# Kernel tuning notes

Hardware: AMD Instinct MI355X
Metric: run time of the kernel (lower is better)

The kernel has to match this reference:

```python
import jax, jax.numpy as jnp
import numpy as np

N_NODES = 100000
N_EDGES = 1600000
F_IN = 128
HID = 128
N_GRAPHS = 1024


def setup_inputs() -> dict:
    key = jax.random.key(0)
    ks = jax.random.split(key, 20)
    x = jax.random.normal(ks[0], (N_NODES, F_IN), dtype=jnp.float32)
    edge_index = jax.random.randint(ks[1], (2, N_EDGES), 0, N_NODES, dtype=jnp.int64)
    batch = jnp.sort(jax.random.randint(ks[2], (N_NODES,), 0, N_GRAPHS, dtype=jnp.int64))
    def lin(k, fi, fo):
        s = 1.0 / np.sqrt(fi)
        return jax.random.uniform(k, (fi, fo), jnp.float32, -s, s)
    params = {
        'W1': lin(ks[3], F_IN, HID), 'b1': jnp.zeros((HID,), jnp.float32),
        'W2': lin(ks[4], HID, HID), 'b2': jnp.zeros((HID,), jnp.float32),
        'W3': lin(ks[5], HID, HID), 'b3': jnp.zeros((HID,), jnp.float32),
        'W4': lin(ks[6], HID, HID), 'b4': jnp.zeros((HID,), jnp.float32),
        'W5': lin(ks[7], HID, HID), 'b5': jnp.zeros((HID,), jnp.float32),
        'beta1': jnp.ones((1,), jnp.float32),
        'beta2': jnp.ones((1,), jnp.float32),
        'Wl': lin(ks[8], HID, 1), 'bl': jnp.zeros((1,), jnp.float32),
    }
    return {'x': x, 'edge_index': edge_index, 'batch': batch, **params}


def _forward(x, src, dst, batch, W1, b1, W2, b2, W3, b3, W4, b4, W5, b5, beta1, beta2, Wl, bl):
    N = x.shape[0]
    # symmetric GCN normalization over A + I (shared by all GCNConv layers)
    deg = jax.ops.segment_sum(jnp.ones_like(dst, dtype=x.dtype), dst, num_segments=N)
    d_is = jnp.where(deg > 0, jax.lax.rsqrt(deg), 0.0)
    norm = d_is[src] * d_is[dst]  # [E+N]

    def gcn(h, W, b):
        m = (h @ W)[src] * norm[:, None]          # per-edge messages
        return jax.ops.segment_sum(m, dst, num_segments=N) + b

    def agnn(h, beta):
        nrm = jnp.maximum(jnp.linalg.norm(h, axis=1, keepdims=True), 1e-12)
        hn = h / nrm
        alpha = beta[0] * jnp.sum(hn[src] * hn[dst], axis=1)  # cosine sim per edge
        amax = jax.ops.segment_max(alpha, dst, num_segments=N)
        e = jnp.exp(alpha - amax[dst])
        denom = jax.ops.segment_sum(e, dst, num_segments=N)
        w = e / denom[dst]
        return jax.ops.segment_sum(h[src] * w[:, None], dst, num_segments=N)

    h = jnp.tanh(gcn(x, W1, b1))
    h = jnp.tanh(gcn(h, W2, b2))
    h = jnp.tanh(gcn(h, W3, b3))
    h = jnp.tanh(gcn(h, W4, b4))
    h = jnp.tanh(gcn(h, W5, b5))
    h = jnp.tanh(agnn(h, beta1))
    h = jnp.tanh(agnn(h, beta2))

    # global mean pool per graph
    sums = jax.ops.segment_sum(h, batch, num_segments=N_GRAPHS)
    cnts = jax.ops.segment_sum(jnp.ones((N,), h.dtype), batch, num_segments=N_GRAPHS)
    pooled = sums / jnp.maximum(cnts, 1.0)[:, None]

    # layer_norm over feature dim, no affine
    mu = jnp.mean(pooled, axis=-1, keepdims=True)
    var = jnp.mean(jnp.square(pooled - mu), axis=-1, keepdims=True)
    ln = (pooled - mu) * jax.lax.rsqrt(var + 1e-5)
    # dropout is identity in eval mode
    return ln @ Wl + bl


def reference(x, edge_index, batch, W1, b1, W2, b2, W3, b3, W4, b4, W5, b5, beta1, beta2, Wl, bl):
    N = x.shape[0]
    loops = jnp.arange(N, dtype=edge_index.dtype)
    src = jnp.concatenate([edge_index[0], loops])  # add self-loops (GCNConv & AGNNConv default)
    dst = jnp.concatenate([edge_index[1], loops])
    return _forward(x, src, dst, batch, W1, b1, W2, b2, W3, b3, W4, b4, W5, b5, beta1, beta2, Wl, bl)
```

## Files before the change

### kernel.cpp

```cpp
#include <hip/hip_runtime.h>
#include <hip/hip_fp16.h>
#include <math.h>

typedef _Float16 f16x8 __attribute__((ext_vector_type(8)));
typedef _Float16 f16x2 __attribute__((ext_vector_type(2)));
typedef float f32x4 __attribute__((ext_vector_type(4)));

union U4H8 { uint4 u; f16x8 h; };
union U4D2 { uint4 u; f16x2 d2[4]; unsigned w[4]; };

__device__ __forceinline__ float fmamix_lo(unsigned pk, float s, float acc) {
    asm("v_fma_mix_f32 %0, %1, %2, %0 op_sel:[0,0,0] op_sel_hi:[1,0,0]"
        : "+v"(acc) : "v"(pk), "v"(s));
    return acc;
}
__device__ __forceinline__ float fmamix_hi(unsigned pk, float s, float acc) {
    asm("v_fma_mix_f32 %0, %1, %2, %0 op_sel:[1,0,0] op_sel_hi:[1,0,0]"
        : "+v"(acc) : "v"(pk), "v"(s));
    return acc;
}
__device__ __forceinline__ float fdot2(f16x2 a, f16x2 b, float c) {
#if __has_builtin(__builtin_amdgcn_fdot2)
    return __builtin_amdgcn_fdot2(a, b, c, false);
#else
    asm("v_dot2_f32_f16 %0, %1, %2, %0" : "+v"(c) : "v"(a), "v"(b));
    return c;
#endif
}

__device__ __forceinline__ void unpack8(uint4 u, float* f) {
    union { uint4 u; __half2 h2[4]; } U; U.u = u;
    float2 a = __half22float2(U.h2[0]);
    float2 b = __half22float2(U.h2[1]);
    float2 c = __half22float2(U.h2[2]);
    float2 d = __half22float2(U.h2[3]);
    f[0] = a.x; f[1] = a.y; f[2] = b.x; f[3] = b.y;
    f[4] = c.x; f[5] = c.y; f[6] = d.x; f[7] = d.y;
}

__global__ void k_zero(int* p, int n) {
    int i = blockIdx.x * blockDim.x + threadIdx.x;
    if (i < n) p[i] = 0;
}

__global__ void k_count(const int* __restrict__ dst, int* deg4, int* rank, int E, int N) {
    int i = blockIdx.x * blockDim.x + threadIdx.x;
    if (i < E) rank[i] = atomicAdd(&deg4[(i & 3) * N + dst[i]], 1);
}

__global__ void k_meta_pre(const int* __restrict__ deg4, int* deg, float* dis, int N) {
    int n = blockIdx.x * blockDim.x + threadIdx.x;
    if (n >= N) return;
    int d = deg4[n] + deg4[N + n] + deg4[2 * N + n] + deg4[3 * N + n];
    deg[n] = d;
    dis[n] = rsqrtf((float)(d + 1));
}

__global__ void k_meta_post(const int* __restrict__ deg4, const int* __restrict__ offs,
                            int4* meta, int N) {
    int n = blockIdx.x * blockDim.x + threadIdx.x;
    if (n >= N) return;
    int d0 = deg4[n], d1 = deg4[N + n], d2 = deg4[2 * N + n];
    meta[n] = make_int4(offs[n] + 1, d0, d0 + d1, d0 + d1 + d2);
}

__global__ void k_scan1(const int* __restrict__ deg, int* part, int N) {
    int base = blockIdx.x * 1024;
    int tid = threadIdx.x;
    int s = 0;
#pragma unroll
    for (int j = 0; j < 4; ++j) {
        int idx = base + tid * 4 + j;
        if (idx < N) s += deg[idx] + 1;
    }
    __shared__ int sm[256];
    sm[tid] = s;
    __syncthreads();
    for (int off = 128; off > 0; off >>= 1) {
        if (tid < off) sm[tid] += sm[tid + off];
        __syncthreads();
    }
    if (tid == 0) part[blockIdx.x] = sm[0];
}

__global__ void k_scan2(int* part, int nb, int* offs, int N) {
    if (blockIdx.x == 0 && threadIdx.x == 0) {
        int run = 0;
        for (int b = 0; b < nb; ++b) { int t = part[b]; part[b] = run; run += t; }
        offs[N] = run;
    }
}

__global__ void k_scan3(const int* __restrict__ deg, const int* __restrict__ part,
                        int* offs, int N) {
    __shared__ int sm[256];
    int base = blockIdx.x * 1024;
    int tid = threadIdx.x;
    int a[4];
    int s = 0;
#pragma unroll
    for (int j = 0; j < 4; ++j) {
        int idx = base + tid * 4 + j;
        a[j] = (idx < N) ? (deg[idx] + 1) : 0;
        s += a[j];
    }
    sm[tid] = s;
    __syncthreads();
    for (int off = 1; off < 256; off <<= 1) {
        int v = (tid >= off) ? sm[tid - off] : 0;
        __syncthreads();
        sm[tid] += v;
        __syncthreads();
    }
    int excl = sm[tid] - s + part[blockIdx.x];
#pragma unroll
    for (int j = 0; j < 4; ++j) {
        int idx = base + tid * 4 + j;
        if (idx < N) offs[idx] = excl;
        excl += a[j];
    }
}

__global__ void k_fill(const int* __restrict__ ei, int E, int N,
                       const int4* __restrict__ meta,
                       const int* __restrict__ rank, int* csr) {
    int i = blockIdx.x * blockDim.x + threadIdx.x;
    if (i < E) {
        int s = ei[i], d = ei[E + i];
        int c = i & 3;
        int4 m = meta[d];
        int base = (c == 0) ? 0 : ((c == 1) ? m.y : ((c == 2) ? m.z : m.w));
        csr[m.x + base + rank[i]] = s;
    } else if (i < E + N) {
        int n = i - E;
        csr[meta[n].x - 1] = n;
    }
}

__global__ void k_gstart(const int* __restrict__ batch, int N, int* gstart, int G) {
    int g = blockIdx.x * blockDim.x + threadIdx.x;
    if (g > G) return;
    int lo = 0, hi = N;
    while (lo < hi) {
        int mid = (lo + hi) >> 1;
        if (batch[mid] < g) lo = mid + 1; else hi = mid;
    }
    gstart[g] = lo;
}

__global__ __launch_bounds__(256) void k_cast(
    const float* __restrict__ x, const float* __restrict__ dis,
    __half* __restrict__ hx, int npairs)
{
    int i = blockIdx.x * blockDim.x + threadIdx.x;
    if (i >= npairs) return;
    float2 v = ((const float2*)x)[i];
    float d = dis[i >> 6];
    ((__half2*)hx)[i] = __floats2half2_rn(d * v.x, d * v.y);
}

__global__ void k_prepw(const float* __restrict__ W, __half* __restrict__ wt_hi,
                        __half* __restrict__ wt_lo) {
    int t = blockIdx.x * 256 + threadIdx.x;
    int j = t & 7, q = t >> 3;
    int l15 = q & 15, nt = (q >> 4) & 7;
    int lg = (q >> 7) & 3, ks = q >> 9;
    int n = nt * 16 + l15, k = ks * 32 + lg * 8 + j;
    float w = W[k * 128 + n];
    __half hi = __float2half_rn(w);
    wt_hi[t] = hi;
    wt_lo[t] = __float2half_rn(w - __half2float(hi));
}

__global__ __launch_bounds__(256) void k_gcn_agg(
    const __half* __restrict__ g, const int* __restrict__ csr,
    const int* __restrict__ offs, const float* __restrict__ dis,
    __half* __restrict__ agg, int N)
{
    int node = (blockIdx.x * blockDim.x + threadIdx.x) >> 4;
    int l = threadIdx.x & 15;
    if (node >= N) return;
    int j0 = offs[node], j1 = offs[node + 1];
    float dd = dis[node];
    const uint4* h4 = (const uint4*)g;
    float one = 1.0f;
    float acc[8] = {0.f, 0.f, 0.f, 0.f, 0.f, 0.f, 0.f, 0.f};
    int j = j0;
    for (; j + 8 <= j1; j += 8) {
        U4D2 u[8];
#pragma unroll
        for (int e = 0; e < 8; ++e) {
            int s = csr[j + e];
            u[e].u = h4[(unsigned)(s * 16 + l)];
        }
#pragma unroll
        for (int e = 0; e < 8; ++e)
#pragma unroll
            for (int k = 0; k < 4; ++k) {
                acc[2 * k]     = fmamix_lo(u[e].w[k], one, acc[2 * k]);
                acc[2 * k + 1] = fmamix_hi(u[e].w[k], one, acc[2 * k + 1]);
            }
    }
    for (; j + 4 <= j1; j += 4) {
        U4D2 u[4];
#pragma unroll
        for (int e = 0; e < 4; ++e) {
            int s = csr[j + e];
            u[e].u = h4[(unsigned)(s * 16 + l)];
        }
#pragma unroll
        for (int e = 0; e < 4; ++e)
#pragma unroll
            for (int k = 0; k < 4; ++k) {
                acc[2 * k]     = fmamix_lo(u[e].w[k], one, acc[2 * k]);
                acc[2 * k + 1] = fmamix_hi(u[e].w[k], one, acc[2 * k + 1]);
            }
    }
    for (; j < j1; ++j) {
        int s = csr[j];
        U4D2 u; u.u = h4[(unsigned)(s * 16 + l)];
#pragma unroll
        for (int k = 0; k < 4; ++k) {
            acc[2 * k]     = fmamix_lo(u.w[k], one, acc[2 * k]);
            acc[2 * k + 1] = fmamix_hi(u.w[k], one, acc[2 * k + 1]);
        }
    }
    union { uint4 u; __half2 h2[4]; } P;
    P.h2[0] = __floats2half2_rn(dd * acc[0], dd * acc[1]);
    P.h2[1] = __floats2half2_rn(dd * acc[2], dd * acc[3]);
    P.h2[2] = __floats2half2_rn(dd * acc[4], dd * acc[5]);
    P.h2[3] = __floats2half2_rn(dd * acc[6], dd * acc[7]);
    ((uint4*)agg)[(unsigned)(node * 16 + l)] = P.u;
}

#define GEMM_STG_OFF 65536
#define GEMM_STG_STRIDE 72
#define GEMM_LDS_BYTES (65536 + 8 * 16 * GEMM_STG_STRIDE)

__global__ __launch_bounds__(512) void k_gemm_mfma(
    const __half* __restrict__ in, const __half* __restrict__ wt_hi,
    const __half* __restrict__ wt_lo, const float* __restrict__ bias,
    const float* __restrict__ scale, __half* __restrict__ out,
    int ntiles, int nrows, float* __restrict__ invn_out)
{
    extern __shared__ char smem[];
    uint4* wlds = (uint4*)smem;
    int tid = threadIdx.x;
    int wv = tid >> 6;
    char* stg = smem + GEMM_STG_OFF + wv * 16 * GEMM_STG_STRIDE;

    {
        const uint4* sh = (const uint4*)wt_hi;
        const uint4* sl = (const uint4*)wt_lo;
        for (int t = tid; t < 2048; t += 512) {
            wlds[t] = sh[t];
            wlds[t + 2048] = sl[t];
        }
    }
    __syncthreads();

    int lane = tid & 63;
    int l15 = lane & 15, lg = lane >> 4;

    f32x4 bv[8];
#pragma unroll
    for (int nt = 0; nt < 8; ++nt)
        bv[nt] = *(const f32x4*)(bias + nt * 16 + lg * 4);

    int wid = blockIdx.x * 8 + wv;
    int t0 = wid * 2;
    for (int tile = t0; tile < t0 + 2 && tile < ntiles; ++tile) {
        int row0 = tile * 16;
        int row = row0 + l15;
        if (row >= nrows) row = nrows - 1;

        U4H8 b[4];
        const uint4* ap = (const uint4*)(in + (size_t)row * 128);
#pragma unroll
        for (int ks = 0; ks < 4; ++ks) b[ks].u = ap[ks * 4 + lg];

        f32x4 acc[8];
#pragma unroll
        for (int nt = 0; nt < 8; ++nt) acc[nt] = (f32x4){0.f, 0.f, 0.f, 0.f};

#pragma unroll
        for (int ks = 0; ks < 4; ++ks) {
#pragma unroll
            for (int nt = 0; nt < 8; ++nt) {
                int fi = (ks * 4 + lg) * 128 + nt * 16 + l15;
                U4H8 ah; ah.u = wlds[fi];
                U4H8 al; al.u = wlds[fi + 2048];
                acc[nt] = __builtin_amdgcn_mfma_f32_16x16x32_f16(ah.h, b[ks].h, acc[nt], 0, 0, 0);
                acc[nt] = __builtin_amdgcn_mfma_f32_16x16x32_f16(al.h, b[ks].h, acc[nt], 0, 0, 0);
            }
        }

        float sc = scale ? scale[row] : 1.0f;
        float sq = 0.f;
        int node = lane >> 2, sub = lane & 3;
#pragma unroll
        for (int np = 0; np < 4; ++np) {
#pragma unroll
            for (int h = 0; h < 2; ++h) {
                int nt = np * 2 + h;
                float o[4];
#pragma unroll
                for (int r = 0; r < 4; ++r) {
                    float xv = acc[nt][r] + bv[nt][r];
                    float e = __expf(xv + xv);
                    o[r] = 1.f - 2.f / (e + 1.f);
                    sq += o[r] * o[r];
                }
                union { __half2 h2[2]; uint2 u; } pk;
                pk.h2[0] = __floats2half2_rn(sc * o[0], sc * o[1]);
                pk.h2[1] = __floats2half2_rn(sc * o[2], sc * o[3]);
                *(uint2*)(stg + l15 * GEMM_STG_STRIDE + h * 32 + lg * 8) = pk.u;
            }
            uint4 v = *(const uint4*)(stg + node * GEMM_STG_STRIDE + sub * 16);
            if (row0 + node < nrows)
                *(uint4*)(out + (size_t)(row0 + node) * 128 + np * 32 + sub * 8) = v;
        }
        if (invn_out) {
            sq += __shfl_xor(sq, 16, 64);
            sq += __shfl_xor(sq, 32, 64);
            if (lg == 0) invn_out[row] = 1.0f / fmaxf(sqrtf(sq), 1e-12f);
        }
    }
}

__global__ __launch_bounds__(256) void k_agnn(
    const __half* __restrict__ h, const int* __restrict__ csr,
    const int* __restrict__ offs, const float* __restrict__ invn,
    const float* __restrict__ beta_p, __half* __restrict__ out, int N,
    float* __restrict__ invn_out)
{
    int node = (blockIdx.x * blockDim.x + threadIdx.x) >> 4;
    int l = threadIdx.x & 15;
    if (node >= N) return;
    int j0 = offs[node], j1 = offs[node + 1];
    const uint4* h4 = (const uint4*)h;
    U4D2 D; D.u = h4[(unsigned)(node * 16 + l)];
    float bi = beta_p[0] * invn[node];
    float denom = 0.f;
    float acc[8] = {0.f, 0.f, 0.f, 0.f, 0.f, 0.f, 0.f, 0.f};
    int j = j0;
    for (; j + 4 <= j1; j += 4) {
        U4D2 A[4];
        float in_[4];
#pragma unroll
        for (int e = 0; e < 4; ++e) {
            int s = csr[j + e];
            in_[e] = invn[s];
            A[e].u = h4[(unsigned)(s * 16 + l)];
        }
        float d[4] = {0.f, 0.f, 0.f, 0.f};
#pragma unroll
        for (int e = 0; e < 4; ++e)
#pragma unroll
            for (int k = 0; k < 4; ++k) d[e] = fdot2(A[e].d2[k], D.d2[k], d[e]);
#pragma unroll
        for (int off = 1; off < 16; off <<= 1) {
            d[0] += __shfl_xor(d[0], off, 64);
            d[1] += __shfl_xor(d[1], off, 64);
            d[2] += __shfl_xor(d[2], off, 64);
            d[3] += __shfl_xor(d[3], off, 64);
        }
        float p[4];
#pragma unroll
        for (int e = 0; e < 4; ++e) {
            p[e] = __expf(bi * in_[e] * d[e]);
            denom += p[e];
        }
#pragma unroll
        for (int e = 0; e < 4; ++e)
#pragma unroll
            for (int k = 0; k < 4; ++k) {
                acc[2 * k]     = fmamix_lo(A[e].w[k], p[e], acc[2 * k]);
                acc[2 * k + 1] = fmamix_hi(A[e].w[k], p[e], acc[2 * k + 1]);
            }
    }
    for (; j < j1; ++j) {
        int s = csr[j];
        float ins = invn[s];
        U4D2 A; A.u = h4[(unsigned)(s * 16 + l)];
        float d = 0.f;
#pragma unroll
        for (int k = 0; k < 4; ++k) d = fdot2(A.d2[k], D.d2[k], d);
#pragma unroll
        for (int off = 1; off < 16; off <<= 1) d += __shfl_xor(d, off, 64);
        float p = __expf(bi * ins * d);
        denom += p;
#pragma unroll
        for (int k = 0; k < 4; ++k) {
            acc[2 * k]     = fmamix_lo(A.w[k], p, acc[2 * k]);
            acc[2 * k + 1] = fmamix_hi(A.w[k], p, acc[2 * k + 1]);
        }
    }
    float inv = 1.0f / denom;
    float o[8];
#pragma unroll
    for (int i = 0; i < 8; ++i) o[i] = tanhf(acc[i] * inv);
    union { uint4 u; __half2 h2[4]; } P;
    P.h2[0] = __floats2half2_rn(o[0], o[1]);
    P.h2[1] = __floats2half2_rn(o[2], o[3]);
    P.h2[2] = __floats2half2_rn(o[4], o[5]);
    P.h2[3] = __floats2half2_rn(o[6], o[7]);
    ((uint4*)out)[(unsigned)(node * 16 + l)] = P.u;
    if (invn_out) {
        float s2 = 0.f;
#pragma unroll
        for (int i = 0; i < 8; ++i) s2 += o[i] * o[i];
#pragma unroll
        for (int off = 1; off < 16; off <<= 1) s2 += __shfl_xor(s2, off, 64);
        if (l == 0) invn_out[node] = 1.0f / fmaxf(sqrtf(s2), 1e-12f);
    }
}

__global__ __launch_bounds__(256) void k_pool(
    const __half* __restrict__ h, const int* __restrict__ gstart,
    const float* __restrict__ Wl, const float* __restrict__ bl,
    float* __restrict__ out, int G)
{
    int g = (blockIdx.x * blockDim.x + threadIdx.x) >> 4;
    int l = threadIdx.x & 15;
    if (g >= G) return;
    int s = gstart[g], e = gstart[g + 1];
    const uint4* hp = (const uint4*)h + l;
    float acc[8] = {0.f, 0.f, 0.f, 0.f, 0.f, 0.f, 0.f, 0.f};
    for (int n = s; n < e; ++n) {
        float f[8]; unpack8(hp[(size_t)n * 16], f);
#pragma unroll
        for (int i = 0; i < 8; ++i) acc[i] += f[i];
    }
    float inv = 1.0f / fmaxf((float)(e - s), 1.0f);
#pragma unroll
    for (int i = 0; i < 8; ++i) acc[i] *= inv;
    float part = 0.f;
#pragma unroll
    for (int i = 0; i < 8; ++i) part += acc[i];
#pragma unroll
    for (int off = 1; off < 16; off <<= 1) part += __shfl_xor(part, off, 64);
    float mu = part * (1.0f / 128.0f);
    float vpart = 0.f;
#pragma unroll
    for (int i = 0; i < 8; ++i) { float d = acc[i] - mu; vpart += d * d; }
#pragma unroll
    for (int off = 1; off < 16; off <<= 1) vpart += __shfl_xor(vpart, off, 64);
    float r = rsqrtf(vpart * (1.0f / 128.0f) + 1e-5f);
    float4 w0 = *(const float4*)(Wl + l * 8);
    float4 w1 = *(const float4*)(Wl + l * 8 + 4);
    float wv[8] = {w0.x, w0.y, w0.z, w0.w, w1.x, w1.y, w1.z, w1.w};
    float dot = 0.f;
#pragma unroll
    for (int i = 0; i < 8; ++i) dot += (acc[i] - mu) * r * wv[i];
#pragma unroll
    for (int off = 1; off < 16; off <<= 1) dot += __shfl_xor(dot, off, 64);
    if (l == 0) out[g] = dot + bl[0];
}

extern "C" void kernel_launch(void* const* d_in, const int* in_sizes, int n_in,
                              void* d_out, int out_size, void* d_ws, size_t ws_size,
                              hipStream_t stream) {
    const float* x  = (const float*)d_in[0];
    const int* ei   = (const int*)d_in[1];
    const int* batch = (const int*)d_in[2];
    const float* Ws[5] = {(const float*)d_in[3], (const float*)d_in[5],
                          (const float*)d_in[7], (const float*)d_in[9],
                          (const float*)d_in[11]};
    const float* bs[5] = {(const float*)d_in[4], (const float*)d_in[6],
                          (const float*)d_in[8], (const float*)d_in[10],
                          (const float*)d_in[12]};
    const float* beta1 = (const float*)d_in[13];
    const float* beta2 = (const float*)d_in[14];
    const float* Wl = (const float*)d_in[15];
    const float* bl = (const float*)d_in[16];
    float* out = (float*)d_out;

    int N = in_sizes[0] / 128;
    int E = in_sizes[1] / 2;
    int G = out_size;

    char* ws = (char*)d_ws;
    size_t off = 0;
    auto alloc = [&](size_t bytes) -> void* {
        void* p = ws + off;
        off = (off + bytes + 255) & ~(size_t)255;
        return p;
    };
    __half* aggh = (__half*)alloc((size_t)N * 128 * 2);
    __half* hA   = (__half*)alloc((size_t)N * 128 * 2);
    __half* hB   = (__half*)alloc((size_t)N * 128 * 2);
    int*   deg4  = (int*)alloc((size_t)4 * N * 4);
    int*   deg   = (int*)alloc((size_t)N * 4);
    int*   offs  = (int*)alloc((size_t)(N + 1) * 4);
    int4*  meta  = (int4*)alloc((size_t)N * 16);
    int*   rank  = (int*)alloc((size_t)E * 4);
    int*   csr   = (int*)alloc((size_t)(E + N) * 4);
    float* dis   = (float*)alloc((size_t)N * 4);
    float* invn  = (float*)alloc((size_t)N * 4);
    float* invn2 = (float*)alloc((size_t)N * 4);
    __half* wtHi = (__half*)alloc((size_t)5 * 16384 * 2);
    __half* wtLo = (__half*)alloc((size_t)5 * 16384 * 2);
    int nb = (N + 1023) / 1024;
    int*   part  = (int*)alloc((size_t)nb * 4);
    int*   gst   = (int*)alloc((size_t)(G + 1) * 4);

    k_zero<<<(4 * N + 255) / 256, 256, 0, stream>>>(deg4, 4 * N);
    k_count<<<(E + 255) / 256, 256, 0, stream>>>(ei + E, deg4, rank, E, N);
    k_meta_pre<<<(N + 255) / 256, 256, 0, stream>>>(deg4, deg, dis, N);
    k_scan1<<<nb, 256, 0, stream>>>(deg, part, N);
    k_scan2<<<1, 64, 0, stream>>>(part, nb, offs, N);
    k_scan3<<<nb, 256, 0, stream>>>(deg, part, offs, N);
    k_meta_post<<<(N + 255) / 256, 256, 0, stream>>>(deg4, offs, meta, N);
    k_fill<<<(E + N + 255) / 256, 256, 0, stream>>>(ei, E, N, meta, rank, csr);
    k_gstart<<<(G + 1 + 255) / 256, 256, 0, stream>>>(batch, N, gst, G);
    k_cast<<<(N * 64 + 255) / 256, 256, 0, stream>>>(x, dis, hA, N * 64);
    for (int l = 0; l < 5; ++l)
        k_prepw<<<64, 256, 0, stream>>>(Ws[l], wtHi + l * 16384, wtLo + l * 16384);

    int aggBlocks = (N + 15) / 16;
    int ntiles = (N + 15) / 16;
    int gemmBlocks = (ntiles + 15) / 16;

    const __half* hin = hA;
    __half* hout = hB;
    for (int l = 0; l < 5; ++l) {
        k_gcn_agg<<<aggBlocks, 256, 0, stream>>>(hin, csr, offs, dis, aggh, N);
        k_gemm_mfma<<<gemmBlocks, 512, GEMM_LDS_BYTES, stream>>>(
            aggh, wtHi + l * 16384, wtLo + l * 16384, bs[l],
            (l < 4) ? dis : nullptr, hout, ntiles, N,
            (l == 4) ? invn : nullptr);
        const __half* t = hin; hin = hout; hout = (__half*)t;
    }
    k_agnn<<<aggBlocks, 256, 0, stream>>>(hin, csr, offs, invn, beta1, hout, N, invn2);
    k_agnn<<<aggBlocks, 256, 0, stream>>>(hout, csr, offs, invn2, beta2, (__half*)hin, N, nullptr);
    k_pool<<<(G + 15) / 16, 256, 0, stream>>>(hin, gst, Wl, bl, out, G);
}
```

Before: 725.1 us.

## Fuse GCN neighbor aggregation into the MFMA GEMM kernel

```diff
diff --git a/kernel.cpp b/kernel.cpp
--- a/kernel.cpp
+++ b/kernel.cpp
@@ -172,76 +172,16 @@
     wt_lo[t] = __float2half_rn(w - __half2float(hi));
 }
 
-__global__ __launch_bounds__(256) void k_gcn_agg(
-    const __half* __restrict__ g, const int* __restrict__ csr,
-    const int* __restrict__ offs, const float* __restrict__ dis,
-    __half* __restrict__ agg, int N)
-{
-    int node = (blockIdx.x * blockDim.x + threadIdx.x) >> 4;
-    int l = threadIdx.x & 15;
-    if (node >= N) return;
-    int j0 = offs[node], j1 = offs[node + 1];
-    float dd = dis[node];
-    const uint4* h4 = (const uint4*)g;
-    float one = 1.0f;
-    float acc[8] = {0.f, 0.f, 0.f, 0.f, 0.f, 0.f, 0.f, 0.f};
-    int j = j0;
-    for (; j + 8 <= j1; j += 8) {
-        U4D2 u[8];
-#pragma unroll
-        for (int e = 0; e < 8; ++e) {
-            int s = csr[j + e];
-            u[e].u = h4[(unsigned)(s * 16 + l)];
-        }
-#pragma unroll
-        for (int e = 0; e < 8; ++e)
-#pragma unroll
-            for (int k = 0; k < 4; ++k) {
-                acc[2 * k]     = fmamix_lo(u[e].w[k], one, acc[2 * k]);
-                acc[2 * k + 1] = fmamix_hi(u[e].w[k], one, acc[2 * k + 1]);
-            }
-    }
-    for (; j + 4 <= j1; j += 4) {
-        U4D2 u[4];
-#pragma unroll
-        for (int e = 0; e < 4; ++e) {
-            int s = csr[j + e];
-            u[e].u = h4[(unsigned)(s * 16 + l)];
-        }
-#pragma unroll
-        for (int e = 0; e < 4; ++e)
-#pragma unroll
-            for (int k = 0; k < 4; ++k) {
-                acc[2 * k]     = fmamix_lo(u[e].w[k], one, acc[2 * k]);
-                acc[2 * k + 1] = fmamix_hi(u[e].w[k], one, acc[2 * k + 1]);
-            }
-    }
-    for (; j < j1; ++j) {
-        int s = csr[j];
-        U4D2 u; u.u = h4[(unsigned)(s * 16 + l)];
-#pragma unroll
-        for (int k = 0; k < 4; ++k) {
-            acc[2 * k]     = fmamix_lo(u.w[k], one, acc[2 * k]);
-            acc[2 * k + 1] = fmamix_hi(u.w[k], one, acc[2 * k + 1]);
-        }
-    }
-    union { uint4 u; __half2 h2[4]; } P;
-    P.h2[0] = __floats2half2_rn(dd * acc[0], dd * acc[1]);
-    P.h2[1] = __floats2half2_rn(dd * acc[2], dd * acc[3]);
-    P.h2[2] = __floats2half2_rn(dd * acc[4], dd * acc[5]);
-    P.h2[3] = __floats2half2_rn(dd * acc[6], dd * acc[7]);
-    ((uint4*)agg)[(unsigned)(node * 16 + l)] = P.u;
-}
-
 #define GEMM_STG_OFF 65536
 #define GEMM_STG_STRIDE 72
 #define GEMM_LDS_BYTES (65536 + 8 * 16 * GEMM_STG_STRIDE)
 
-__global__ __launch_bounds__(512) void k_gemm_mfma(
-    const __half* __restrict__ in, const __half* __restrict__ wt_hi,
-    const __half* __restrict__ wt_lo, const float* __restrict__ bias,
-    const float* __restrict__ scale, __half* __restrict__ out,
-    int ntiles, int nrows, float* __restrict__ invn_out)
+__global__ __launch_bounds__(512) void k_gcn_fused(
+    const __half* __restrict__ h, const int* __restrict__ csr,
+    const int* __restrict__ offs, const float* __restrict__ dis,
+    const __half* __restrict__ wt_hi, const __half* __restrict__ wt_lo,
+    const float* __restrict__ bias, const float* __restrict__ scale,
+    __half* __restrict__ out, int ntiles, int nrows, float* __restrict__ invn_out)
 {
     extern __shared__ char smem[];
     uint4* wlds = (uint4*)smem;
@@ -261,6 +201,8 @@
 
     int lane = tid & 63;
     int l15 = lane & 15, lg = lane >> 4;
+    const uint4* h4 = (const uint4*)h;
+    float one = 1.0f;
 
     f32x4 bv[8];
 #pragma unroll
@@ -274,15 +216,55 @@
         int row = row0 + l15;
         if (row >= nrows) row = nrows - 1;
 
+        float ag[32];
+#pragma unroll
+        for (int i = 0; i < 32; ++i) ag[i] = 0.f;
+        int j0 = offs[row], j1 = offs[row + 1];
+        int j = j0;
+        for (; j + 2 <= j1; j += 2) {
+            int s0 = csr[j], s1 = csr[j + 1];
+            U4D2 c0[4], c1[4];
+#pragma unroll
+            for (int ks = 0; ks < 4; ++ks) c0[ks].u = h4[(unsigned)(s0 * 16 + ks * 4 + lg)];
+#pragma unroll
+            for (int ks = 0; ks < 4; ++ks) c1[ks].u = h4[(unsigned)(s1 * 16 + ks * 4 + lg)];
+#pragma unroll
+            for (int ks = 0; ks < 4; ++ks)
+#pragma unroll
+                for (int w = 0; w < 4; ++w) {
+                    ag[ks * 8 + 2 * w]     = fmamix_lo(c0[ks].w[w], one, ag[ks * 8 + 2 * w]);
+                    ag[ks * 8 + 2 * w + 1] = fmamix_hi(c0[ks].w[w], one, ag[ks * 8 + 2 * w + 1]);
+                    ag[ks * 8 + 2 * w]     = fmamix_lo(c1[ks].w[w], one, ag[ks * 8 + 2 * w]);
+                    ag[ks * 8 + 2 * w + 1] = fmamix_hi(c1[ks].w[w], one, ag[ks * 8 + 2 * w + 1]);
+                }
+        }
+        for (; j < j1; ++j) {
+            int s = csr[j];
+            U4D2 c[4];
+#pragma unroll
+            for (int ks = 0; ks < 4; ++ks) c[ks].u = h4[(unsigned)(s * 16 + ks * 4 + lg)];
+#pragma unroll
+            for (int ks = 0; ks < 4; ++ks)
+#pragma unroll
+                for (int w = 0; w < 4; ++w) {
+                    ag[ks * 8 + 2 * w]     = fmamix_lo(c[ks].w[w], one, ag[ks * 8 + 2 * w]);
+                    ag[ks * 8 + 2 * w + 1] = fmamix_hi(c[ks].w[w], one, ag[ks * 8 + 2 * w + 1]);
+                }
+        }
+        float dd = dis[row];
         U4H8 b[4];
-        const uint4* ap = (const uint4*)(in + (size_t)row * 128);
-#pragma unroll
-        for (int ks = 0; ks < 4; ++ks) b[ks].u = ap[ks * 4 + lg];
+#pragma unroll
+        for (int ks = 0; ks < 4; ++ks) {
+            union { uint4 u; __half2 h2[4]; } P;
+#pragma unroll
+            for (int w = 0; w < 4; ++w)
+                P.h2[w] = __floats2half2_rn(dd * ag[ks * 8 + 2 * w], dd * ag[ks * 8 + 2 * w + 1]);
+            b[ks].u = P.u;
+        }
 
         f32x4 acc[8];
 #pragma unroll
         for (int nt = 0; nt < 8; ++nt) acc[nt] = (f32x4){0.f, 0.f, 0.f, 0.f};
-
 #pragma unroll
         for (int ks = 0; ks < 4; ++ks) {
 #pragma unroll
@@ -301,8 +283,8 @@
 #pragma unroll
         for (int np = 0; np < 4; ++np) {
 #pragma unroll
-            for (int h = 0; h < 2; ++h) {
-                int nt = np * 2 + h;
+            for (int hh = 0; hh < 2; ++hh) {
+                int nt = np * 2 + hh;
                 float o[4];
 #pragma unroll
                 for (int r = 0; r < 4; ++r) {
@@ -314,7 +296,7 @@
                 union { __half2 h2[2]; uint2 u; } pk;
                 pk.h2[0] = __floats2half2_rn(sc * o[0], sc * o[1]);
                 pk.h2[1] = __floats2half2_rn(sc * o[2], sc * o[3]);
-                *(uint2*)(stg + l15 * GEMM_STG_STRIDE + h * 32 + lg * 8) = pk.u;
+                *(uint2*)(stg + l15 * GEMM_STG_STRIDE + hh * 32 + lg * 8) = pk.u;
             }
             uint4 v = *(const uint4*)(stg + node * GEMM_STG_STRIDE + sub * 16);
             if (row0 + node < nrows)
@@ -487,7 +469,6 @@
         off = (off + bytes + 255) & ~(size_t)255;
         return p;
     };
-    __half* aggh = (__half*)alloc((size_t)N * 128 * 2);
     __half* hA   = (__half*)alloc((size_t)N * 128 * 2);
     __half* hB   = (__half*)alloc((size_t)N * 128 * 2);
     int*   deg4  = (int*)alloc((size_t)4 * N * 4);
@@ -520,14 +501,13 @@
 
     int aggBlocks = (N + 15) / 16;
     int ntiles = (N + 15) / 16;
-    int gemmBlocks = (ntiles + 15) / 16;
+    int fusedBlocks = (ntiles + 15) / 16;
 
     const __half* hin = hA;
     __half* hout = hB;
     for (int l = 0; l < 5; ++l) {
-        k_gcn_agg<<<aggBlocks, 256, 0, stream>>>(hin, csr, offs, dis, aggh, N);
-        k_gemm_mfma<<<gemmBlocks, 512, GEMM_LDS_BYTES, stream>>>(
-            aggh, wtHi + l * 16384, wtLo + l * 16384, bs[l],
+        k_gcn_fused<<<fusedBlocks, 512, GEMM_LDS_BYTES, stream>>>(
+            hin, csr, offs, dis, wtHi + l * 16384, wtLo + l * 16384, bs[l],
             (l < 4) ? dis : nullptr, hout, ntiles, N,
             (l == 4) ? invn : nullptr);
         const __half* t = hin; hin = hout; hout = (__half*)t;
```

Measured after the change: 736.9 us. Within noise of the previous version (+1.6%).
